# Kernel tuning notes

Measured on AMD Instinct MI355X. Metric: run time of the kernel, lower is better.

## Reference

```python
import jax, jax.numpy as jnp
import numpy as np

D_MODEL = 2048
NUM_HEADS = 16
HEAD_DIM = D_MODEL // NUM_HEADS
ENTROPY_THRESHOLD = 0.01
B, T = 4, 2048


def setup_inputs() -> dict:
    key = jax.random.key(0)
    ks = jax.random.split(key, 10)
    s = 1.0 / np.sqrt(D_MODEL)
    inp = {
        "x": jax.random.normal(ks[0], (B, T, D_MODEL), dtype=jnp.float32),
        "mask": jnp.ones((B, T), dtype=jnp.int32),
        "Wq": jax.random.uniform(ks[1], (D_MODEL, D_MODEL), jnp.float32, -s, s),
        "bq": jax.random.uniform(ks[2], (D_MODEL,), jnp.float32, -s, s),
        "Wk": jax.random.uniform(ks[3], (D_MODEL, D_MODEL), jnp.float32, -s, s),
        "bk": jax.random.uniform(ks[4], (D_MODEL,), jnp.float32, -s, s),
        "Wv": jax.random.uniform(ks[5], (D_MODEL, D_MODEL), jnp.float32, -s, s),
        "bv": jax.random.uniform(ks[6], (D_MODEL,), jnp.float32, -s, s),
        "Wo": jax.random.uniform(ks[7], (D_MODEL, D_MODEL), jnp.float32, -s, s),
        "bo": jax.random.uniform(ks[8], (D_MODEL,), jnp.float32, -s, s),
    }
    return inp


def reference(x, mask, Wq, bq, Wk, bk, Wv, bv, Wo, bo):
    Bx, Tx, C = x.shape

    def heads(y):  # (B,T,C) -> (B,H,T,hd)
        return y.reshape(Bx, Tx, NUM_HEADS, HEAD_DIM).transpose(0, 2, 1, 3)

    q = heads(x @ Wq.T + bq)
    k = heads(x @ Wk.T + bk)
    v = heads(x @ Wv.T + bv)

    scores = jnp.einsum("bhqd,bhkd->bhqk", q, k) / np.sqrt(HEAD_DIM).astype(np.float32)
    scores = jnp.where(mask[:, None, None, :] == 0, -jnp.inf, scores)
    weights = jax.nn.softmax(scores, axis=-1)

    # entropy reduction (eval mode: conditional dropout is identity, so ent
    # does not alter the output, but we compute it faithfully)
    ent = -jnp.sum(weights * jnp.log(weights + 1e-9), axis=-1).mean()
    weights = jnp.where(ent < ENTROPY_THRESHOLD, weights, weights)  # dropout(p=0.1, training=False) == identity

    attended = jnp.einsum("bhqk,bhkd->bhqd", weights, v)
    attended = attended.transpose(0, 2, 1, 3).reshape(Bx, Tx, C)
    return attended @ Wo.T + bo
```

## Files before the change

### kernel.cpp

```cpp
#include <hip/hip_runtime.h>
#include <cstdint>
#include <cstddef>

#define D_MODEL 2048
#define T_SEQ   2048
#define N_BATCH 4
#define N_HEAD  16
#define HD      128
#define M_ROWS  (N_BATCH * T_SEQ)
#define N_QKV   (3 * D_MODEL)

typedef short          s8x  __attribute__((ext_vector_type(8)));
typedef float          f4x  __attribute__((ext_vector_type(4)));
typedef float          f4v  __attribute__((ext_vector_type(4)));
typedef unsigned short u16;
typedef u16            u16x8 __attribute__((ext_vector_type(8)));

__device__ __forceinline__ u16 f2bf(float f) {
    union { float f; unsigned u; } v; v.f = f;
    unsigned r = (v.u + 0x7FFFu + ((v.u >> 16) & 1u)) >> 16;
    return (u16)r;
}

__device__ __forceinline__ void glds16(const void* g, void* l) {
    __builtin_amdgcn_global_load_lds(
        (const __attribute__((address_space(1))) void*)g,
        (__attribute__((address_space(3))) void*)l, 16, 0, 0);
}

__global__ void cvt_f32_bf16(const float* __restrict__ in, u16* __restrict__ out, int n8) {
    int i = blockIdx.x * blockDim.x + threadIdx.x;
    int stride = gridDim.x * blockDim.x;
    for (; i < n8; i += stride) {
        f4v a = reinterpret_cast<const f4v*>(in)[2 * i];
        f4v b = reinterpret_cast<const f4v*>(in)[2 * i + 1];
        u16x8 o;
        o[0] = f2bf(a[0]); o[1] = f2bf(a[1]); o[2] = f2bf(a[2]); o[3] = f2bf(a[3]);
        o[4] = f2bf(b[0]); o[5] = f2bf(b[1]); o[6] = f2bf(b[2]); o[7] = f2bf(b[3]);
        reinterpret_cast<u16x8*>(out)[i] = o;
    }
}

template<bool OUT_BF16>
__global__ __launch_bounds__(256)
void gemm_bt(const u16* __restrict__ A, const u16* __restrict__ B,
             const float* __restrict__ bias, void* __restrict__ C,
             int M, int N, int K, int nbn) {
    __shared__ u16 As[128 * 32];
    __shared__ u16 Bs[128 * 32];

    int nwg = gridDim.x;
    int wg  = blockIdx.x;
    int qx  = nwg >> 3;
    wg = (wg & 7) * qx + (wg >> 3);
    int bm = wg / nbn, bn = wg % nbn;

    int t   = threadIdx.x;
    int wid = t >> 6;
    int l15 = t & 15, l4 = (t >> 4) & 3;
    int wr  = wid >> 1, wc = wid & 1;

    f4x acc[4][4] = {};

    const u16* ga = A + (size_t)(bm * 128 + (t >> 2)) * K + (t & 3) * 8;
    const u16* gb = B + (size_t)(bn * 128 + (t >> 2)) * K + (t & 3) * 8;
    char* lA = (char*)As + wid * 1024;
    char* lB = (char*)Bs + wid * 1024;

    for (int k0 = 0; k0 < K; k0 += 32) {
        glds16(ga,              lA);
        glds16(ga + 64 * (size_t)K, lA + 4096);
        glds16(gb,              lB);
        glds16(gb + 64 * (size_t)K, lB + 4096);
        ga += 32; gb += 32;
        __syncthreads();

        s8x af[4], bfr[4];
        #pragma unroll
        for (int m = 0; m < 4; m++) {
            af[m]  = *reinterpret_cast<const s8x*>(As + (wr * 64 + m * 16 + l15) * 32 + l4 * 8);
            bfr[m] = *reinterpret_cast<const s8x*>(Bs + (wc * 64 + m * 16 + l15) * 32 + l4 * 8);
        }
        #pragma unroll
        for (int m = 0; m < 4; m++)
            #pragma unroll
            for (int n = 0; n < 4; n++)
                acc[m][n] = __builtin_amdgcn_mfma_f32_16x16x32_bf16(af[m], bfr[n], acc[m][n], 0, 0, 0);
        __syncthreads();
    }

    int row0 = bm * 128 + wr * 64;
    int col0 = bn * 128 + wc * 64;
    #pragma unroll
    for (int n = 0; n < 4; n++) {
        int col = col0 + n * 16 + l15;
        float bv = bias[col];
        #pragma unroll
        for (int m = 0; m < 4; m++) {
            #pragma unroll
            for (int r = 0; r < 4; r++) {
                int row = row0 + m * 16 + l4 * 4 + r;
                float v = acc[m][n][r] + bv;
                if (OUT_BF16) ((u16*)C)[(size_t)row * N + col]   = f2bf(v);
                else          ((float*)C)[(size_t)row * N + col] = v;
            }
        }
    }
}

__global__ __launch_bounds__(256)
void attn(const u16* __restrict__ qkv, const int* __restrict__ mask,
          u16* __restrict__ att) {
    __shared__ u16  Ks[64 * 128];
    __shared__ u16  Vt[128 * 72];
    __shared__ u16  Pl[4][32 * 72];
    __shared__ float mb[64];

    int wg = blockIdx.x;
    int q8 = gridDim.x >> 3;
    wg = (wg & 7) * q8 + (wg >> 3);
    int bh = wg >> 4;
    int qb = wg & 15;
    int b  = bh >> 4, h = bh & 15;

    int t = threadIdx.x, wid = t >> 6;
    int lane = t & 63, l15 = lane & 15, l4 = lane >> 4;

    const size_t rs = N_QKV;
    const u16* qbase = qkv + (size_t)(b * T_SEQ) * rs;
    const u16* kbase = qbase + D_MODEL + h * HD;
    const u16* vbase = qbase + 2 * D_MODEL + h * HD;

    s8x qf[2][4];
    #pragma unroll
    for (int ms = 0; ms < 2; ms++)
        #pragma unroll
        for (int kk = 0; kk < 4; kk++) {
            int row = qb * 128 + wid * 32 + ms * 16 + l15;
            qf[ms][kk] = *reinterpret_cast<const s8x*>(
                qbase + (size_t)row * rs + h * HD + kk * 32 + l4 * 8);
        }

    f4x acc[2][8] = {};
    float mrun[2][4], lrun[2][4];
    #pragma unroll
    for (int ms = 0; ms < 2; ms++)
        #pragma unroll
        for (int r = 0; r < 4; r++) { mrun[ms][r] = -__builtin_inff(); lrun[ms][r] = 0.f; }

    const float cs = 0.08838834764831845f * 1.4426950408889634f;

    int vp = t & 31;
    int vs = t >> 5;
    u16* Pw = Pl[wid];

    for (int kv0 = 0; kv0 < T_SEQ; kv0 += 64) {
        {
            int krow = t >> 4, s = t & 15;
            #pragma unroll
            for (int i = 0; i < 4; i++) {
                int row = i * 16 + krow;
                const u16* src = kbase + (size_t)(kv0 + row) * rs + ((s ^ (row & 7)) * 8);
                glds16(src, (char*)Ks + i * 4096 + wid * 1024);
            }
        }
        s8x v0a = *reinterpret_cast<const s8x*>(vbase + (size_t)(kv0 + 2 * vp) * rs + vs * 16);
        s8x v0b = *reinterpret_cast<const s8x*>(vbase + (size_t)(kv0 + 2 * vp) * rs + vs * 16 + 8);
        s8x v1a = *reinterpret_cast<const s8x*>(vbase + (size_t)(kv0 + 2 * vp + 1) * rs + vs * 16);
        s8x v1b = *reinterpret_cast<const s8x*>(vbase + (size_t)(kv0 + 2 * vp + 1) * rs + vs * 16 + 8);
        if (t < 64) mb[t] = mask[b * T_SEQ + kv0 + t] ? 0.f : -__builtin_inff();
        #pragma unroll
        for (int j = 0; j < 8; j++) {
            unsigned w0 = (u16)v0a[j] | ((unsigned)(u16)v1a[j] << 16);
            *reinterpret_cast<unsigned*>(&Vt[(vs * 16 + j) * 72 + 2 * vp]) = w0;
            unsigned w1 = (u16)v0b[j] | ((unsigned)(u16)v1b[j] << 16);
            *reinterpret_cast<unsigned*>(&Vt[(vs * 16 + 8 + j) * 72 + 2 * vp]) = w1;
        }
        __syncthreads();

        f4x sf[2][4] = {};
        #pragma unroll
        for (int t4 = 0; t4 < 4; t4++) {
            s8x kf[4];
            #pragma unroll
            for (int kk = 0; kk < 4; kk++) {
                int row  = t4 * 16 + l15;
                int slot = (kk * 4 + l4) ^ (row & 7);
                kf[kk] = *reinterpret_cast<const s8x*>(Ks + row * 128 + slot * 8);
            }
            #pragma unroll
            for (int ms = 0; ms < 2; ms++)
                #pragma unroll
                for (int kk = 0; kk < 4; kk++)
                    sf[ms][t4] = __builtin_amdgcn_mfma_f32_16x16x32_bf16(qf[ms][kk], kf[kk], sf[ms][t4], 0, 0, 0);
        }

        float mbv[4];
        #pragma unroll
        for (int t4 = 0; t4 < 4; t4++) mbv[t4] = mb[t4 * 16 + l15];
        #pragma unroll
        for (int ms = 0; ms < 2; ms++)
            #pragma unroll
            for (int t4 = 0; t4 < 4; t4++)
                sf[ms][t4] += mbv[t4];

        #pragma unroll
        for (int ms = 0; ms < 2; ms++) {
            float mx[4];
            #pragma unroll
            for (int r = 0; r < 4; r++) {
                float a0 = fmaxf(fmaxf(sf[ms][0][r], sf[ms][1][r]),
                                 fmaxf(sf[ms][2][r], sf[ms][3][r]));
                #pragma unroll
                for (int sh = 1; sh <= 8; sh <<= 1) a0 = fmaxf(a0, __shfl_xor(a0, sh));
                mx[r] = a0;
            }
            f4x fv; float mc[4];
            #pragma unroll
            for (int r = 0; r < 4; r++) {
                float mn = fmaxf(mrun[ms][r], mx[r]);
                float f  = exp2f((mrun[ms][r] - mn) * cs);
                mrun[ms][r] = mn;
                lrun[ms][r] *= f;
                fv[r] = f;
                mc[r] = mn * cs;
            }
            #pragma unroll
            for (int dt = 0; dt < 8; dt++) acc[ms][dt] *= fv;
            #pragma unroll
            for (int t4 = 0; t4 < 4; t4++) {
                #pragma unroll
                for (int r = 0; r < 4; r++) {
                    float p = exp2f(sf[ms][t4][r] * cs - mc[r]);
                    lrun[ms][r] += p;
                    Pw[(ms * 16 + l4 * 4 + r) * 72 + t4 * 16 + l15] = f2bf(p);
                }
            }
        }
        asm volatile("" ::: "memory");

        s8x pa[2][2];
        #pragma unroll
        for (int ms = 0; ms < 2; ms++)
            #pragma unroll
            for (int ks = 0; ks < 2; ks++)
                pa[ms][ks] = *reinterpret_cast<const s8x*>(Pw + (ms * 16 + l15) * 72 + ks * 32 + l4 * 8);
        #pragma unroll
        for (int dt = 0; dt < 8; dt++) {
            s8x vbf[2];
            #pragma unroll
            for (int ks = 0; ks < 2; ks++)
                vbf[ks] = *reinterpret_cast<const s8x*>(Vt + (dt * 16 + l15) * 72 + ks * 32 + l4 * 8);
            #pragma unroll
            for (int ms = 0; ms < 2; ms++)
                #pragma unroll
                for (int ks = 0; ks < 2; ks++)
                    acc[ms][dt] = __builtin_amdgcn_mfma_f32_16x16x32_bf16(pa[ms][ks], vbf[ks], acc[ms][dt], 0, 0, 0);
        }
        __syncthreads();
    }

    #pragma unroll
    for (int ms = 0; ms < 2; ms++) {
        f4x inv;
        #pragma unroll
        for (int r = 0; r < 4; r++) {
            float s = lrun[ms][r];
            #pragma unroll
            for (int sh = 1; sh <= 8; sh <<= 1) s += __shfl_xor(s, sh);
            inv[r] = 1.f / s;
        }
        #pragma unroll
        for (int dt = 0; dt < 8; dt++) {
            f4x o = acc[ms][dt] * inv;
            #pragma unroll
            for (int r = 0; r < 4; r++) {
                int row = qb * 128 + wid * 32 + ms * 16 + l4 * 4 + r;
                int col = h * HD + dt * 16 + l15;
                att[(size_t)(b * T_SEQ + row) * D_MODEL + col] = f2bf(o[r]);
            }
        }
    }
}

extern "C" void kernel_launch(void* const* d_in, const int* in_sizes, int n_in,
                              void* d_out, int out_size, void* d_ws, size_t ws_size,
                              hipStream_t stream) {
    (void)in_sizes; (void)n_in; (void)out_size; (void)ws_size;

    const float* x    = (const float*)d_in[0];
    const int*   mask = (const int*)d_in[1];
    const float* Wq   = (const float*)d_in[2];
    const float* bq   = (const float*)d_in[3];
    const float* Wk   = (const float*)d_in[4];
    const float* bk   = (const float*)d_in[5];
    const float* Wv   = (const float*)d_in[6];
    const float* bv   = (const float*)d_in[7];
    const float* Wo   = (const float*)d_in[8];
    const float* bo   = (const float*)d_in[9];
    float* out = (float*)d_out;

    char* ws = (char*)d_ws;
    u16*   xb   = (u16*)(ws);
    u16*   wqkv = (u16*)(ws + 33554432);
    u16*   wo   = (u16*)(ws + 58720256);
    float* bqkv = (float*)(ws + 67108864);
    u16*   qkvb = (u16*)(ws + 67133440);
    u16*   attb = (u16*)(ws + 167796736);

    cvt_f32_bf16<<<2048, 256, 0, stream>>>(x,  xb,               16777216 / 8);
    cvt_f32_bf16<<<1024, 256, 0, stream>>>(Wq, wqkv,              4194304 / 8);
    cvt_f32_bf16<<<1024, 256, 0, stream>>>(Wk, wqkv + 4194304,    4194304 / 8);
    cvt_f32_bf16<<<1024, 256, 0, stream>>>(Wv, wqkv + 8388608,    4194304 / 8);
    cvt_f32_bf16<<<1024, 256, 0, stream>>>(Wo, wo,                4194304 / 8);
    hipMemcpyAsync(bqkv,        bq, 2048 * 4, hipMemcpyDeviceToDevice, stream);
    hipMemcpyAsync(bqkv + 2048, bk, 2048 * 4, hipMemcpyDeviceToDevice, stream);
    hipMemcpyAsync(bqkv + 4096, bv, 2048 * 4, hipMemcpyDeviceToDevice, stream);

    gemm_bt<true><<<64 * 48, 256, 0, stream>>>(xb, wqkv, bqkv, qkvb, M_ROWS, N_QKV, D_MODEL, 48);
    attn<<<1024, 256, 0, stream>>>(qkvb, mask, attb);
    gemm_bt<false><<<64 * 16, 256, 0, stream>>>(attb, wo, bo, out, M_ROWS, D_MODEL, D_MODEL, 16);
}
```

Measured before the change: 1.034 ms.

## Double-buffer V tiles, read K from global, fold softmax scale into Q projection

```diff
diff --git a/kernel.cpp b/kernel.cpp
--- a/kernel.cpp
+++ b/kernel.cpp
@@ -26,6 +26,20 @@
     __builtin_amdgcn_global_load_lds(
         (const __attribute__((address_space(1))) void*)g,
         (__attribute__((address_space(3))) void*)l, 16, 0, 0);
+}
+
+template<int CTRL>
+__device__ __forceinline__ float dppror(float v) {
+    int i = __builtin_bit_cast(int, v);
+    int r = __builtin_amdgcn_update_dpp(i, i, CTRL, 0xf, 0xf, true);
+    return __builtin_bit_cast(float, r);
+}
+__device__ __forceinline__ float rowmax16(float v) {
+    v = fmaxf(v, dppror<0x128>(v));
+    v = fmaxf(v, dppror<0x124>(v));
+    v = fmaxf(v, dppror<0x122>(v));
+    v = fmaxf(v, dppror<0x121>(v));
+    return v;
 }
 
 __global__ void cvt_f32_bf16(const float* __restrict__ in, u16* __restrict__ out, int n8) {
@@ -45,7 +59,7 @@
 __global__ __launch_bounds__(256)
 void gemm_bt(const u16* __restrict__ A, const u16* __restrict__ B,
              const float* __restrict__ bias, void* __restrict__ C,
-             int M, int N, int K, int nbn) {
+             int M, int N, int K, int nbn, float qscale, int qcols) {
     __shared__ u16 As[128 * 32];
     __shared__ u16 Bs[128 * 32];
 
@@ -95,12 +109,13 @@
     for (int n = 0; n < 4; n++) {
         int col = col0 + n * 16 + l15;
         float bv = bias[col];
+        float sc = (col < qcols) ? qscale : 1.0f;
         #pragma unroll
         for (int m = 0; m < 4; m++) {
             #pragma unroll
             for (int r = 0; r < 4; r++) {
                 int row = row0 + m * 16 + l4 * 4 + r;
-                float v = acc[m][n][r] + bv;
+                float v = (acc[m][n][r] + bv) * sc;
                 if (OUT_BF16) ((u16*)C)[(size_t)row * N + col]   = f2bf(v);
                 else          ((float*)C)[(size_t)row * N + col] = v;
             }
@@ -108,13 +123,12 @@
     }
 }
 
-__global__ __launch_bounds__(256)
+__global__ __launch_bounds__(256, 2)
 void attn(const u16* __restrict__ qkv, const int* __restrict__ mask,
           u16* __restrict__ att) {
-    __shared__ u16  Ks[64 * 128];
-    __shared__ u16  Vt[128 * 72];
+    __shared__ u16  Vt[2][128 * 72];
     __shared__ u16  Pl[4][32 * 72];
-    __shared__ float mb[64];
+    __shared__ float mbuf[2][64];
 
     int wg = blockIdx.x;
     int q8 = gridDim.x >> 3;
@@ -148,46 +162,44 @@
         #pragma unroll
         for (int r = 0; r < 4; r++) { mrun[ms][r] = -__builtin_inff(); lrun[ms][r] = 0.f; }
 
-    const float cs = 0.08838834764831845f * 1.4426950408889634f;
-
     int vp = t & 31;
     int vs = t >> 5;
     u16* Pw = Pl[wid];
 
-    for (int kv0 = 0; kv0 < T_SEQ; kv0 += 64) {
-        {
-            int krow = t >> 4, s = t & 15;
-            #pragma unroll
-            for (int i = 0; i < 4; i++) {
-                int row = i * 16 + krow;
-                const u16* src = kbase + (size_t)(kv0 + row) * rs + ((s ^ (row & 7)) * 8);
-                glds16(src, (char*)Ks + i * 4096 + wid * 1024);
-            }
-        }
-        s8x v0a = *reinterpret_cast<const s8x*>(vbase + (size_t)(kv0 + 2 * vp) * rs + vs * 16);
-        s8x v0b = *reinterpret_cast<const s8x*>(vbase + (size_t)(kv0 + 2 * vp) * rs + vs * 16 + 8);
-        s8x v1a = *reinterpret_cast<const s8x*>(vbase + (size_t)(kv0 + 2 * vp + 1) * rs + vs * 16);
-        s8x v1b = *reinterpret_cast<const s8x*>(vbase + (size_t)(kv0 + 2 * vp + 1) * rs + vs * 16 + 8);
-        if (t < 64) mb[t] = mask[b * T_SEQ + kv0 + t] ? 0.f : -__builtin_inff();
+    {
+        s8x v0a = *reinterpret_cast<const s8x*>(vbase + (size_t)(2 * vp) * rs + vs * 16);
+        s8x v0b = *reinterpret_cast<const s8x*>(vbase + (size_t)(2 * vp) * rs + vs * 16 + 8);
+        s8x v1a = *reinterpret_cast<const s8x*>(vbase + (size_t)(2 * vp + 1) * rs + vs * 16);
+        s8x v1b = *reinterpret_cast<const s8x*>(vbase + (size_t)(2 * vp + 1) * rs + vs * 16 + 8);
+        if (t < 64) mbuf[0][t] = mask[b * T_SEQ + t] ? 0.f : -__builtin_inff();
         #pragma unroll
         for (int j = 0; j < 8; j++) {
             unsigned w0 = (u16)v0a[j] | ((unsigned)(u16)v1a[j] << 16);
-            *reinterpret_cast<unsigned*>(&Vt[(vs * 16 + j) * 72 + 2 * vp]) = w0;
+            *reinterpret_cast<unsigned*>(&Vt[0][(vs * 16 + j) * 72 + 2 * vp]) = w0;
             unsigned w1 = (u16)v0b[j] | ((unsigned)(u16)v1b[j] << 16);
-            *reinterpret_cast<unsigned*>(&Vt[(vs * 16 + 8 + j) * 72 + 2 * vp]) = w1;
+            *reinterpret_cast<unsigned*>(&Vt[0][(vs * 16 + 8 + j) * 72 + 2 * vp]) = w1;
         }
         __syncthreads();
+    }
+
+    for (int tt = 0; tt < T_SEQ / 64; tt++) {
+        int kv0 = tt * 64;
+        int cur = tt & 1, nxt = cur ^ 1;
+        int kvn = kv0 + 64; if (kvn >= T_SEQ) kvn = 0;
+
+        s8x v0a = *reinterpret_cast<const s8x*>(vbase + (size_t)(kvn + 2 * vp) * rs + vs * 16);
+        s8x v0b = *reinterpret_cast<const s8x*>(vbase + (size_t)(kvn + 2 * vp) * rs + vs * 16 + 8);
+        s8x v1a = *reinterpret_cast<const s8x*>(vbase + (size_t)(kvn + 2 * vp + 1) * rs + vs * 16);
+        s8x v1b = *reinterpret_cast<const s8x*>(vbase + (size_t)(kvn + 2 * vp + 1) * rs + vs * 16 + 8);
 
         f4x sf[2][4] = {};
         #pragma unroll
         for (int t4 = 0; t4 < 4; t4++) {
             s8x kf[4];
             #pragma unroll
-            for (int kk = 0; kk < 4; kk++) {
-                int row  = t4 * 16 + l15;
-                int slot = (kk * 4 + l4) ^ (row & 7);
-                kf[kk] = *reinterpret_cast<const s8x*>(Ks + row * 128 + slot * 8);
-            }
+            for (int kk = 0; kk < 4; kk++)
+                kf[kk] = *reinterpret_cast<const s8x*>(
+                    kbase + (size_t)(kv0 + t4 * 16 + l15) * rs + kk * 32 + l4 * 8);
             #pragma unroll
             for (int ms = 0; ms < 2; ms++)
                 #pragma unroll
@@ -197,7 +209,7 @@
 
         float mbv[4];
         #pragma unroll
-        for (int t4 = 0; t4 < 4; t4++) mbv[t4] = mb[t4 * 16 + l15];
+        for (int t4 = 0; t4 < 4; t4++) mbv[t4] = mbuf[cur][t4 * 16 + l15];
         #pragma unroll
         for (int ms = 0; ms < 2; ms++)
             #pragma unroll
@@ -211,19 +223,17 @@
             for (int r = 0; r < 4; r++) {
                 float a0 = fmaxf(fmaxf(sf[ms][0][r], sf[ms][1][r]),
                                  fmaxf(sf[ms][2][r], sf[ms][3][r]));
-                #pragma unroll
-                for (int sh = 1; sh <= 8; sh <<= 1) a0 = fmaxf(a0, __shfl_xor(a0, sh));
-                mx[r] = a0;
+                mx[r] = rowmax16(a0);
             }
             f4x fv; float mc[4];
             #pragma unroll
             for (int r = 0; r < 4; r++) {
                 float mn = fmaxf(mrun[ms][r], mx[r]);
-                float f  = exp2f((mrun[ms][r] - mn) * cs);
+                float f  = exp2f(mrun[ms][r] - mn);
                 mrun[ms][r] = mn;
                 lrun[ms][r] *= f;
                 fv[r] = f;
-                mc[r] = mn * cs;
+                mc[r] = mn;
             }
             #pragma unroll
             for (int dt = 0; dt < 8; dt++) acc[ms][dt] *= fv;
@@ -231,7 +241,7 @@
             for (int t4 = 0; t4 < 4; t4++) {
                 #pragma unroll
                 for (int r = 0; r < 4; r++) {
-                    float p = exp2f(sf[ms][t4][r] * cs - mc[r]);
+                    float p = exp2f(sf[ms][t4][r] - mc[r]);
                     lrun[ms][r] += p;
                     Pw[(ms * 16 + l4 * 4 + r) * 72 + t4 * 16 + l15] = f2bf(p);
                 }
@@ -250,12 +260,21 @@
             s8x vbf[2];
             #pragma unroll
             for (int ks = 0; ks < 2; ks++)
-                vbf[ks] = *reinterpret_cast<const s8x*>(Vt + (dt * 16 + l15) * 72 + ks * 32 + l4 * 8);
+                vbf[ks] = *reinterpret_cast<const s8x*>(&Vt[cur][(dt * 16 + l15) * 72 + ks * 32 + l4 * 8]);
             #pragma unroll
             for (int ms = 0; ms < 2; ms++)
                 #pragma unroll
                 for (int ks = 0; ks < 2; ks++)
                     acc[ms][dt] = __builtin_amdgcn_mfma_f32_16x16x32_bf16(pa[ms][ks], vbf[ks], acc[ms][dt], 0, 0, 0);
+        }
+
+        if (t < 64) mbuf[nxt][t] = mask[b * T_SEQ + kvn + t] ? 0.f : -__builtin_inff();
+        #pragma unroll
+        for (int j = 0; j < 8; j++) {
+            unsigned w0 = (u16)v0a[j] | ((unsigned)(u16)v1a[j] << 16);
+            *reinterpret_cast<unsigned*>(&Vt[nxt][(vs * 16 + j) * 72 + 2 * vp]) = w0;
+            unsigned w1 = (u16)v0b[j] | ((unsigned)(u16)v1b[j] << 16);
+            *reinterpret_cast<unsigned*>(&Vt[nxt][(vs * 16 + 8 + j) * 72 + 2 * vp]) = w1;
         }
         __syncthreads();
     }
@@ -317,7 +336,9 @@
     hipMemcpyAsync(bqkv + 2048, bk, 2048 * 4, hipMemcpyDeviceToDevice, stream);
     hipMemcpyAsync(bqkv + 4096, bv, 2048 * 4, hipMemcpyDeviceToDevice, stream);
 
-    gemm_bt<true><<<64 * 48, 256, 0, stream>>>(xb, wqkv, bqkv, qkvb, M_ROWS, N_QKV, D_MODEL, 48);
+    const float cs = 0.08838834764831845f * 1.4426950408889634f;
+
+    gemm_bt<true><<<64 * 48, 256, 0, stream>>>(xb, wqkv, bqkv, qkvb, M_ROWS, N_QKV, D_MODEL, 48, cs, D_MODEL);
     attn<<<1024, 256, 0, stream>>>(qkvb, mask, attb);
-    gemm_bt<false><<<64 * 16, 256, 0, stream>>>(attb, wo, bo, out, M_ROWS, D_MODEL, D_MODEL, 16);
-}
+    gemm_bt<false><<<64 * 16, 256, 0, stream>>>(attb, wo, bo, out, M_ROWS, D_MODEL, D_MODEL, 16, 1.0f, 0);
+}
```

Result: faster. 880.9 us (-14.8%).
